# Kernel optimization log

Hardware: AMD Instinct MI355X
Metric: run time of the kernel (lower is better)

## Reference

```python
import jax, jax.numpy as jnp
import numpy as np

K = 7  # window_size from init


def setup_inputs() -> dict:
    key = jax.random.key(0)
    k1, k2, k3 = jax.random.split(key, 3)
    B, S, C, H, W = 2, 5, 256, 200, 200
    hidden = max(C // 16, 4)  # 16
    feats = jax.random.normal(k1, (B, S, C, H, W), dtype=jnp.float32)
    w1 = jax.random.normal(k2, (hidden, C), dtype=jnp.float32) * (1.0 / np.sqrt(C))
    b1 = jnp.zeros((hidden,), dtype=jnp.float32)
    w2 = jax.random.normal(k3, (1, hidden), dtype=jnp.float32) * (1.0 / np.sqrt(hidden))
    b2 = jnp.zeros((1,), dtype=jnp.float32)
    return {"feats": feats, "w1": w1, "b1": b1, "w2": w2, "b2": b2}


def reference(feats, w1, b1, w2, b2):
    B, S, C, H, W = feats.shape
    pad_h = (K - H % K) % K
    pad_w = (K - W % K) % K
    x = jnp.pad(feats, ((0, 0), (0, 0), (0, 0), (0, pad_h), (0, pad_w)))
    Hp, Wp = H + pad_h, W + pad_w
    Hb, Wb = Hp // K, Wp // K
    # windowed view, matching torch unfold(3,k,k).unfold(4,k,k): [B,S,C,Hb,Wb,k,k]
    xw = x.reshape(B, S, C, Hb, K, Wb, K).transpose(0, 1, 2, 3, 5, 4, 6)
    # per-window channel descriptor: mean over the k x k window
    g = xw.mean(axis=(-1, -2))                      # [B,S,C,Hb,Wb]
    g = g.transpose(0, 1, 3, 4, 2)                  # [B,S,Hb,Wb,C]
    h = jax.nn.relu(jnp.einsum('bshwc,dc->bshwd', g, w1) + b1)
    logits = jnp.einsum('bshwd,od->bshwo', h, w2) + b2
    logits = logits[..., 0]                         # [B,S,Hb,Wb]
    # NOTE: faithful to source: softmax over dim=-1 (Wb axis), not the slice axis
    weights = jax.nn.softmax(logits, axis=-1)       # [B,S,Hb,Wb]
    # weighted sum over slices
    fused = jnp.einsum('bschwij,bshw->bchwij', xw, weights)  # [B,C,Hb,Wb,k,k]
    # faithful reassembly: permute(0,1,4,2,5,3) -> [B,C,k,Hb,k,Wb], then reshape
    fused = fused.transpose(0, 1, 4, 2, 5, 3).reshape(B, C, Hp, Wp)
    return fused[:, :, :H, :W]
```

## Files before the change

kernel.cpp:

```cpp
#include <hip/hip_runtime.h>
#include <math.h>

constexpr int B = 2, S = 5, C = 256, H = 200, W = 200;
constexpr int KW = 7;
constexpr int HB = 29, WB = 29;
constexpr int HID = 16;
constexpr int NW = HB * WB;

__global__ __launch_bounds__(512) void k_winsum(const float* __restrict__ feats,
                                                float* __restrict__ gsum) {
    const int blk = (int)blockIdx.x;
    const float* src = feats + (size_t)blk * (H * W);

    __shared__ float colg[HB * W];

    const int tid = (int)threadIdx.x;

    for (int q = tid; q < HB * (W / 4); q += 512) {
        int hb = q / (W / 4);
        int x4 = q - hb * (W / 4);
        int y0 = hb * KW;
        float4 a = make_float4(0.f, 0.f, 0.f, 0.f);
#pragma unroll
        for (int i = 0; i < KW; ++i) {
            int y = y0 + i;
            if (y < H) {
                float4 v = ((const float4*)(src + (size_t)y * W))[x4];
                a.x += v.x; a.y += v.y; a.z += v.z; a.w += v.w;
            }
        }
        ((float4*)(colg + hb * W))[x4] = a;
    }
    __syncthreads();

    float* dst = gsum + (size_t)blk * NW;
    for (int p = tid; p < NW; p += 512) {
        int hb = p / WB;
        int wb = p - hb * WB;
        int x0 = wb * KW;
        float s = 0.f;
#pragma unroll
        for (int j = 0; j < KW; ++j) {
            int x = x0 + j;
            if (x < W) s += colg[hb * W + x];
        }
        dst[p] = s;
    }
}

__global__ __launch_bounds__(256) void k_weights(const float* __restrict__ gsum,
                                                 const float* __restrict__ w1,
                                                 const float* __restrict__ b1,
                                                 const float* __restrict__ w2,
                                                 const float* __restrict__ b2,
                                                 float* __restrict__ weights) {
    int blk = blockIdx.x;
    int hb = blk % HB; blk /= HB;
    int s  = blk % S;
    int b  = blk / S;
    const int bs = b * S + s;

    __shared__ float w1s[HID * C];
    __shared__ float part[8 * HID * WB];
    __shared__ float lg[WB];

    const int tid = (int)threadIdx.x;
    for (int i = tid; i < HID * C; i += 256) w1s[i] = w1[i];
    __syncthreads();

    if (tid < 8 * WB) {
        const int cg = tid / WB;
        const int wb = tid - cg * WB;
        float acc[HID];
#pragma unroll
        for (int d = 0; d < HID; ++d) acc[d] = 0.f;
        const float* g = gsum + (size_t)bs * C * NW + hb * WB + wb;
        const int c0 = cg * (C / 8);
#pragma unroll 4
        for (int c = c0; c < c0 + C / 8; ++c) {
            float gc = g[(size_t)c * NW];
#pragma unroll
            for (int d = 0; d < HID; ++d) acc[d] += gc * w1s[d * C + c];
        }
#pragma unroll
        for (int d = 0; d < HID; ++d) part[(cg * HID + d) * WB + wb] = acc[d];
    }
    __syncthreads();

    if (tid < WB) {
        float logit = b2[0];
#pragma unroll
        for (int d = 0; d < HID; ++d) {
            float a = 0.f;
#pragma unroll
            for (int cg = 0; cg < 8; ++cg) a += part[(cg * HID + d) * WB + tid];
            float h = a * (1.0f / 49.0f) + b1[d];
            logit += fmaxf(h, 0.0f) * w2[d];
        }
        lg[tid] = logit;
    }
    __syncthreads();
    if (tid < WB) {
        float m = -INFINITY;
        for (int t = 0; t < WB; ++t) m = fmaxf(m, lg[t]);
        float sum = 0.f;
        for (int t = 0; t < WB; ++t) sum += expf(lg[t] - m);
        weights[(size_t)bs * NW + hb * WB + tid] = expf(lg[tid] - m) / sum;
    }
}

__global__ __launch_bounds__(512) void k_fuse(const float* __restrict__ feats,
                                              const float* __restrict__ weights,
                                              float* __restrict__ out) {
    int blk = blockIdx.x;
    const int hb = blk % HB; blk /= HB;
    const int c  = (C - 1) - (blk % C);
    const int b  = (B - 1) - (blk / C);

    __shared__ float buf[S][KW * W];
    __shared__ float wsl[S][WB];

    const int tid = (int)threadIdx.x;
    const size_t plane = (size_t)H * W;
    const size_t sstride = (size_t)C * plane;
    const float* f0 = feats + ((size_t)b * S * C + c) * plane;
    const int y_in0 = hb * KW;

    for (int q = tid; q < S * 350; q += 512) {
        int s = q / 350;
        int r = q - s * 350;
        int i = r / 50;
        float4 v = make_float4(0.f, 0.f, 0.f, 0.f);
        if (y_in0 + i < H)
            v = ((const float4*)(f0 + (size_t)s * sstride + (size_t)y_in0 * W))[r];
        ((float4*)&buf[s][0])[r] = v;
    }
    if (tid < S * WB) {
        int s  = tid / WB;
        int wb = tid - s * WB;
        wsl[s][wb] = weights[((size_t)((b * S + s) * HB + hb)) * WB + wb];
    }
    __syncthreads();

    float* o = out + ((size_t)b * C + c) * plane;
    for (int p = tid; p < KW * 50; p += 512) {
        int i = p / 50;
        int y = i * HB + hb;
        if (y < H) {
            int x0 = (p - i * 50) * 4;
            float4 r4;
            float* rp = (float*)&r4;
#pragma unroll
            for (int u = 0; u < 4; ++u) {
                int x  = x0 + u;
                int j  = x / WB;
                int wb = x - j * WB;
                int x_in = wb * KW + j;
                float acc = 0.f;
                if (x_in < W) {
#pragma unroll
                    for (int s = 0; s < S; ++s)
                        acc += buf[s][i * W + x_in] * wsl[s][wb];
                }
                rp[u] = acc;
            }
            ((float4*)(o + (size_t)y * W))[x0 / 4] = r4;
        }
    }
}

extern "C" void kernel_launch(void* const* d_in, const int* in_sizes, int n_in,
                              void* d_out, int out_size, void* d_ws, size_t ws_size,
                              hipStream_t stream) {
    const float* feats = (const float*)d_in[0];
    const float* w1    = (const float*)d_in[1];
    const float* b1    = (const float*)d_in[2];
    const float* w2    = (const float*)d_in[3];
    const float* b2    = (const float*)d_in[4];
    float* out = (float*)d_out;

    float* gsum    = (float*)d_ws;
    float* weights = gsum + (size_t)B * S * C * NW;

    hipLaunchKernelGGL(k_winsum, dim3(B * S * C), dim3(512), 0, stream, feats, gsum);
    hipLaunchKernelGGL(k_weights, dim3(B * S * HB), dim3(256), 0, stream,
                       gsum, w1, b1, w2, b2, weights);
    hipLaunchKernelGGL(k_fuse, dim3(B * C * HB), dim3(512), 0, stream,
                       feats, weights, out);
}
```

Before: 172.5 us.

## Loop k_fuse over bands per block with register-staged double buffering

k_fuse now launches one block per (batch, channel) and iterates over all 29 row bands. The next band is prefetched into registers while the current band is computed from shared memory, then stored into the alternate LDS buffer. All window weights are loaded once per block. This removes per-block launch and weight-load overhead, but it cuts the grid to 512 blocks and raises LDS use, which limits memory-level parallelism for a bandwidth-bound kernel.

Result: slower. 187.3 us (+8.6%).

```diff
diff --git a/kernel.cpp b/kernel.cpp
--- a/kernel.cpp
+++ b/kernel.cpp
@@ -109,63 +109,90 @@
     }
 }
 
+__device__ __forceinline__ void load_band(const float* __restrict__ f0,
+                                          size_t sstride, int hb, int tid,
+                                          float4* regs) {
+#pragma unroll
+    for (int k = 0; k < 4; ++k) {
+        int q = k * 512 + tid;
+        regs[k] = make_float4(0.f, 0.f, 0.f, 0.f);
+        if (q < S * 350) {
+            int s = q / 350, r = q - s * 350;
+            int i = r / 50;
+            int y = hb * KW + i;
+            if (y < H)
+                regs[k] = ((const float4*)(f0 + (size_t)s * sstride +
+                                           (size_t)y * W))[r - i * 50];
+        }
+    }
+}
+
+__device__ __forceinline__ void store_band(float* __restrict__ bufp, int tid,
+                                           const float4* regs) {
+#pragma unroll
+    for (int k = 0; k < 4; ++k) {
+        int q = k * 512 + tid;
+        if (q < S * 350) {
+            ((float4*)bufp)[q] = regs[k];
+        }
+    }
+}
+
 __global__ __launch_bounds__(512) void k_fuse(const float* __restrict__ feats,
                                               const float* __restrict__ weights,
                                               float* __restrict__ out) {
-    int blk = blockIdx.x;
-    const int hb = blk % HB; blk /= HB;
-    const int c  = (C - 1) - (blk % C);
-    const int b  = (B - 1) - (blk / C);
-
-    __shared__ float buf[S][KW * W];
-    __shared__ float wsl[S][WB];
+    const int c = (C - 1) - ((int)blockIdx.x % C);
+    const int b = (B - 1) - ((int)blockIdx.x / C);
+
+    __shared__ float buf[2][S][KW * W];
+    __shared__ float wsl[S][NW];
 
     const int tid = (int)threadIdx.x;
     const size_t plane = (size_t)H * W;
     const size_t sstride = (size_t)C * plane;
     const float* f0 = feats + ((size_t)b * S * C + c) * plane;
-    const int y_in0 = hb * KW;
-
-    for (int q = tid; q < S * 350; q += 512) {
-        int s = q / 350;
-        int r = q - s * 350;
-        int i = r / 50;
-        float4 v = make_float4(0.f, 0.f, 0.f, 0.f);
-        if (y_in0 + i < H)
-            v = ((const float4*)(f0 + (size_t)s * sstride + (size_t)y_in0 * W))[r];
-        ((float4*)&buf[s][0])[r] = v;
-    }
-    if (tid < S * WB) {
-        int s  = tid / WB;
-        int wb = tid - s * WB;
-        wsl[s][wb] = weights[((size_t)((b * S + s) * HB + hb)) * WB + wb];
-    }
-    __syncthreads();
-
     float* o = out + ((size_t)b * C + c) * plane;
-    for (int p = tid; p < KW * 50; p += 512) {
-        int i = p / 50;
-        int y = i * HB + hb;
-        if (y < H) {
-            int x0 = (p - i * 50) * 4;
-            float4 r4;
-            float* rp = (float*)&r4;
-#pragma unroll
-            for (int u = 0; u < 4; ++u) {
-                int x  = x0 + u;
-                int j  = x / WB;
-                int wb = x - j * WB;
-                int x_in = wb * KW + j;
-                float acc = 0.f;
-                if (x_in < W) {
-#pragma unroll
-                    for (int s = 0; s < S; ++s)
-                        acc += buf[s][i * W + x_in] * wsl[s][wb];
+
+    for (int q = tid; q < S * NW; q += 512)
+        ((float*)wsl)[q] = weights[(size_t)b * S * NW + q];
+
+    float4 r0[4];
+    load_band(f0, sstride, 0, tid, r0);
+    store_band(&buf[0][0][0], tid, r0);
+    __syncthreads();
+
+    for (int hb = 0; hb < HB; ++hb) {
+        const int cur = hb & 1;
+        float4 rn[4];
+        if (hb + 1 < HB) load_band(f0, sstride, hb + 1, tid, rn);
+
+        if (tid < 350) {
+            int i  = tid / 50;
+            int y  = i * HB + hb;
+            if (y < H) {
+                int x0 = (tid - i * 50) * 4;
+                float4 acc4;
+                float* ap = (float*)&acc4;
+#pragma unroll
+                for (int u = 0; u < 4; ++u) {
+                    int x  = x0 + u;
+                    int j  = x / WB;
+                    int wb = x - j * WB;
+                    int x_in = wb * KW + j;
+                    float acc = 0.f;
+                    if (x_in < W) {
+#pragma unroll
+                        for (int s = 0; s < S; ++s)
+                            acc += buf[cur][s][i * W + x_in] * wsl[s][hb * WB + wb];
+                    }
+                    ap[u] = acc;
                 }
-                rp[u] = acc;
+                ((float4*)(o + (size_t)y * W))[x0 / 4] = acc4;
             }
-            ((float4*)(o + (size_t)y * W))[x0 / 4] = r4;
-        }
+        }
+
+        if (hb + 1 < HB) store_band(&buf[cur ^ 1][0][0], tid, rn);
+        __syncthreads();
     }
 }
 
@@ -185,6 +212,6 @@
     hipLaunchKernelGGL(k_winsum, dim3(B * S * C), dim3(512), 0, stream, feats, gsum);
     hipLaunchKernelGGL(k_weights, dim3(B * S * HB), dim3(256), 0, stream,
                        gsum, w1, b1, w2, b2, weights);
-    hipLaunchKernelGGL(k_fuse, dim3(B * C * HB), dim3(512), 0, stream,
+    hipLaunchKernelGGL(k_fuse, dim3(B * C), dim3(512), 0, stream,
                        feats, weights, out);
 }
```
